# Performance work log

Measured on AMD Instinct MI355X. Metric: run time of the kernel, lower is better.

The kernel has to match this reference:

```python
import jax, jax.numpy as jnp
import numpy as np

B, S, D, H, L, V = 2, 2048, 1024, 16, 4, 2000
DK = D // H
DFF = 4 * D
EPS = 1e-5


def _pos_encoding(s, d):
    pos = np.arange(s, dtype=np.float64)[:, None]
    i = np.arange(d, dtype=np.float64)[None, :]
    angle = pos / np.power(10000.0, (i - (i % 2)) / d)
    pe = np.where(i % 2 == 0, np.sin(angle), np.cos(angle))
    return jnp.asarray(pe, jnp.float32)  # [S, D]


def setup_inputs() -> dict:
    key = jax.random.key(0)
    ks = jax.random.split(key, 12)
    sc = 0.02
    return {
        "indices": jax.random.randint(ks[0], (B, S), 0, V),
        "emb": jax.random.normal(ks[1], (V, D), jnp.float32) * sc,
        "Wq": jax.random.normal(ks[2], (L, H, DK, D), jnp.float32) * sc,
        "Wk": jax.random.normal(ks[3], (L, H, DK, D), jnp.float32) * sc,
        "Wv": jax.random.normal(ks[4], (L, H, DK, D), jnp.float32) * sc,
        "Wo": jax.random.normal(ks[5], (L, D, D), jnp.float32) * sc,
        "ln1_w": jnp.ones((L, D), jnp.float32),
        "ln1_b": jnp.zeros((L, D), jnp.float32),
        "W1": jax.random.normal(ks[6], (L, DFF, D), jnp.float32) * sc,
        "W2": jax.random.normal(ks[7], (L, D, DFF), jnp.float32) * sc,
        "ln2_w": jnp.ones((L, D), jnp.float32),
        "ln2_b": jnp.zeros((L, D), jnp.float32),
        "Wout": jax.random.normal(ks[8], (V, D), jnp.float32) * sc,
    }


def _layernorm(x, w, b):
    m = jnp.mean(x, axis=-1, keepdims=True)
    v = jnp.mean(jnp.square(x - m), axis=-1, keepdims=True)
    return (x - m) * jax.lax.rsqrt(v + EPS) * w + b


def reference(indices, emb, Wq, Wk, Wv, Wo, ln1_w, ln1_b, W1, W2, ln2_w, ln2_b, Wout):
    x = emb[indices] + _pos_encoding(S, D)  # [B, S, D]
    causal = jnp.tril(jnp.ones((S, S), bool))
    inv_sqrt_dk = 1.0 / np.sqrt(DK)
    for l in range(L):
        # per-head QKV projections, vectorized over heads
        q = jnp.einsum("bsd,hkd->bhsk", x, Wq[l])
        k = jnp.einsum("bsd,hkd->bhsk", x, Wk[l])
        v = jnp.einsum("bsd,hkd->bhsk", x, Wv[l])
        scores = jnp.einsum("bhqk,bhmk->bhqm", q, k) * inv_sqrt_dk
        scores = jnp.where(causal, scores, -jnp.inf)
        attn = jax.nn.softmax(scores, axis=-1)
        o = jnp.einsum("bhqm,bhmk->bhqk", attn, v)
        o = o.transpose(0, 2, 1, 3).reshape(B, S, D)  # concat heads
        o = o @ Wo[l].T
        x = _layernorm(x + o, ln1_w[l], ln1_b[l])
        h = jax.nn.relu(x @ W1[l].T) @ W2[l].T
        x = _layernorm(x + h, ln2_w[l], ln2_b[l])
    return x @ Wout.T  # [B, S, V]
```

## Files before the change

kernel.cpp:

```cpp
#include <hip/hip_runtime.h>
#include <hip/hip_bf16.h>

#define B_   2
#define S_   2048
#define D_   1024
#define H_   16
#define L_   4
#define DK_  64
#define DFF_ 4096
#define V_   2000

typedef __bf16 bf16x8 __attribute__((ext_vector_type(8)));
typedef float  f32x4  __attribute__((ext_vector_type(4)));
typedef __attribute__((address_space(1))) const void* as1cv;
typedef __attribute__((address_space(3))) void* as3v;

__device__ __forceinline__ void async_copy16(const void* g, void* l) {
    __builtin_amdgcn_global_load_lds((as1cv)g, (as3v)l, 16, 0, 0);
}

__global__ __launch_bounds__(256)
void canon_k(const void* __restrict__ src, __hip_bfloat16* __restrict__ dst,
             long n, const unsigned short* __restrict__ probe)
{
    const bool isbf = (probe[0] == 0x3F80u);
    long i0 = ((long)blockIdx.x * 256 + threadIdx.x) * 8;
    if (isbf) {
        const __hip_bfloat16* s = (const __hip_bfloat16*)src;
        #pragma unroll
        for (int j = 0; j < 8; ++j) {
            long i = i0 + j;
            if (i < n) dst[i] = s[i];
        }
    } else {
        const float* s = (const float*)src;
        #pragma unroll
        for (int j = 0; j < 8; ++j) {
            long i = i0 + j;
            if (i < n) dst[i] = __float2bfloat16(s[i]);
        }
    }
}

template<int MODE, int BN = 128>
__global__ __launch_bounds__(256, 2)
void gemm_bt(const __hip_bfloat16* __restrict__ A,
             const __hip_bfloat16* __restrict__ Wa,
             const __hip_bfloat16* __restrict__ Wb,
             const __hip_bfloat16* __restrict__ Wc,
             void* __restrict__ Oa, void* __restrict__ Obp, void* __restrict__ Ocp,
             const __hip_bfloat16* __restrict__ Res,
             const unsigned short* __restrict__ probe,
             int M, int N, int K)
{
    constexpr int NFR = BN / 32;

    const __hip_bfloat16* W = Wa;
    void* Out = Oa;
    if (blockIdx.z == 1) { W = Wb; Out = Obp; }
    else if (blockIdx.z == 2) { W = Wc; Out = Ocp; }

    __shared__ __bf16 As[2][128 * 32];
    __shared__ __bf16 Bs[2][BN * 32];

    const int tid  = threadIdx.x;
    const int wave = tid >> 6;
    const int lane = tid & 63;
    const int quad = lane >> 4;
    const int l16  = lane & 15;
    const int bm = blockIdx.x;
    const int bn = blockIdx.y;
    const int wm = (wave >> 1) * 64;
    const int wn = (wave & 1) * (BN / 2);

    const int sr = tid >> 2;
    const int sc = (tid & 3) * 8;
    const __hip_bfloat16* ap0 = A + (long)(bm * 128 + sr) * K + sc;
    const __hip_bfloat16* ap1 = ap0 + (long)64 * K;
    const __hip_bfloat16* bp0 = W + (long)(bn * BN + sr) * K + sc;
    const __hip_bfloat16* bp1 = bp0 + (long)64 * K;
    const bool bok0 = (bn * BN + sr) < N;
    const bool bok1 = (BN == 128) && (bn * BN + sr + 64) < N;

    if (N % BN) {
        #pragma unroll
        for (int bi = 0; bi < 2; ++bi)
            for (int c = tid; c < BN * 4; c += 256)
                ((bf16x8*)Bs[bi])[c] = (bf16x8)0;
        __syncthreads();
    }

    f32x4 acc[4][NFR] = {};
    const int nsteps = K >> 5;

    async_copy16(ap0, As[0] + wave * 512);
    async_copy16(ap1, As[0] + 2048 + wave * 512);
    if (bok0) async_copy16(bp0, Bs[0] + wave * 512);
    if constexpr (BN == 128) { if (bok1) async_copy16(bp1, Bs[0] + 2048 + wave * 512); }
    __syncthreads();

    int cur = 0;
    for (int t = 0; t < nsteps; ++t) {
        const int nxt = cur ^ 1;
        if (t + 1 < nsteps) {
            const int k0 = (t + 1) << 5;
            async_copy16(ap0 + k0, As[nxt] + wave * 512);
            async_copy16(ap1 + k0, As[nxt] + 2048 + wave * 512);
            if (bok0) async_copy16(bp0 + k0, Bs[nxt] + wave * 512);
            if constexpr (BN == 128) { if (bok1) async_copy16(bp1 + k0, Bs[nxt] + 2048 + wave * 512); }
        }

        bf16x8 af[4], bfr[NFR];
        #pragma unroll
        for (int i = 0; i < 4; ++i)
            af[i] = *(const bf16x8*)(As[cur] + (wm + i * 16 + l16) * 32 + quad * 8);
        #pragma unroll
        for (int i = 0; i < NFR; ++i)
            bfr[i] = *(const bf16x8*)(Bs[cur] + (wn + i * 16 + l16) * 32 + quad * 8);
        #pragma unroll
        for (int i = 0; i < 4; ++i)
            #pragma unroll
            for (int j = 0; j < NFR; ++j)
                acc[i][j] = __builtin_amdgcn_mfma_f32_16x16x32_bf16(af[i], bfr[j], acc[i][j], 0, 0, 0);

        __syncthreads();
        cur = nxt;
    }

    const bool out_bf = (MODE != 1) && (MODE != 3 || probe[0] == 0x3F80u);
    #pragma unroll
    for (int i = 0; i < 4; ++i) {
        #pragma unroll
        for (int r = 0; r < 4; ++r) {
            const long row = bm * 128 + wm + i * 16 + quad * 4 + r;
            #pragma unroll
            for (int j = 0; j < NFR; ++j) {
                const int col = bn * BN + wn + j * 16 + l16;
                if (col < N) {
                    const long idx = row * (long)N + col;
                    float v = acc[i][j][r];
                    if constexpr (MODE == 1) {
                        ((float*)Out)[idx] = v + __bfloat162float(Res[idx]);
                    } else if constexpr (MODE == 2) {
                        ((__hip_bfloat16*)Out)[idx] = __float2bfloat16(v > 0.f ? v : 0.f);
                    } else {
                        if (out_bf) ((__hip_bfloat16*)Out)[idx] = __float2bfloat16(v);
                        else        ((float*)Out)[idx] = v;
                    }
                }
            }
        }
    }
}

__global__ __launch_bounds__(256, 2)
void flash_attn(const __hip_bfloat16* __restrict__ Qg,
                const __hip_bfloat16* __restrict__ Kg,
                const __hip_bfloat16* __restrict__ Vg,
                __hip_bfloat16* __restrict__ Og)
{
    const int gid = blockIdx.x + 16 * (blockIdx.y + 16 * blockIdx.z);
    const int r8   = gid & 7;
    const int q9   = gid >> 3;
    const int bx   = q9 & 15;
    const int grp  = r8 + 8 * (q9 >> 4);
    const int h  = grp & 15;
    const int b  = grp >> 4;

    const int tid  = threadIdx.x;
    const int wave = tid >> 6;
    const int lane = tid & 63;
    const int quad = lane >> 4;
    const int l16  = lane & 15;

    __shared__ __bf16 Qs[64 * 64];
    __shared__ __bf16 Ks[2][64 * 64];
    __shared__ __bf16 Vs[64 * 64];
    __shared__ __bf16 Vt[64 * 72];
    __shared__ __bf16 Ps[4][16 * 72];

    const long base = ((long)b * S_) * D_ + (long)h * DK_;
    const int sr  = tid >> 3;
    const int scq = ((tid & 7) ^ (sr & 7)) * 8;
    const int scv = (tid & 7) * 8;

    for (int pr = 0; pr < 2; ++pr) {
        const int qt = pr ? (31 - bx) : bx;
        const int ntile = qt + 1;

        const __hip_bfloat16* qp = Qg + base + (long)(qt * 64 + sr) * D_ + scq;
        async_copy16(qp,           Qs + wave * 512);
        async_copy16(qp + 32 * D_, Qs + 2048 + wave * 512);
        {
            const __hip_bfloat16* kp = Kg + base + (long)sr * D_ + scq;
            const __hip_bfloat16* vp = Vg + base + (long)sr * D_ + scv;
            async_copy16(kp,           Ks[0] + wave * 512);
            async_copy16(kp + 32 * D_, Ks[0] + 2048 + wave * 512);
            async_copy16(vp,           Vs + wave * 512);
            async_copy16(vp + 32 * D_, Vs + 2048 + wave * 512);
        }
        __syncthreads();

        const int qr = wave * 16 + l16;
        const __bf16* qrow = Qs + qr * 64;
        bf16x8 qf0 = *(const bf16x8*)(qrow + (( quad      ^ (qr & 7)) * 8));
        bf16x8 qf1 = *(const bf16x8*)(qrow + (((quad + 4) ^ (qr & 7)) * 8));
        #pragma unroll
        for (int j = 0; j < 8; ++j) {
            qf0[j] = (__bf16)((float)qf0[j] * 0.125f);
            qf1[j] = (__bf16)((float)qf1[j] * 0.125f);
        }

        f32x4 o_acc[4] = {};
        float m_run[4], l_run[4];
        #pragma unroll
        for (int rr = 0; rr < 4; ++rr) { m_run[rr] = -1e30f; l_run[rr] = 0.f; }

        const int q_base = qt * 64 + wave * 16 + quad * 4;

        for (int it = 0; it < ntile; ++it) {
            const int cur = it & 1;
            const int kv0 = it * 64;
            const bool more = (it + 1 < ntile);

            if (more) {
                const __hip_bfloat16* kp = Kg + base + (long)(kv0 + 64 + sr) * D_ + scq;
                async_copy16(kp,           Ks[cur ^ 1] + wave * 512);
                async_copy16(kp + 32 * D_, Ks[cur ^ 1] + 2048 + wave * 512);
            }

            #pragma unroll
            for (int i = 0; i < 2; ++i) {
                const int seg = i * 256 + tid;
                const int dk  = seg & 63;
                const int kvc = (seg >> 6) * 8;
                bf16x8 t;
                #pragma unroll
                for (int j = 0; j < 8; ++j) t[j] = Vs[(kvc + j) * 64 + dk];
                *(bf16x8*)(Vt + dk * 72 + kvc) = t;
            }

            f32x4 sAcc[4] = {};
            #pragma unroll
            for (int nt = 0; nt < 4; ++nt) {
                const int kr = nt * 16 + l16;
                const __bf16* krow = Ks[cur] + kr * 64;
                const bf16x8 kf0 = *(const bf16x8*)(krow + (( quad      ^ (kr & 7)) * 8));
                const bf16x8 kf1 = *(const bf16x8*)(krow + (((quad + 4) ^ (kr & 7)) * 8));
                sAcc[nt] = __builtin_amdgcn_mfma_f32_16x16x32_bf16(qf0, kf0, sAcc[nt], 0, 0, 0);
                sAcc[nt] = __builtin_amdgcn_mfma_f32_16x16x32_bf16(qf1, kf1, sAcc[nt], 0, 0, 0);
            }

            float rmax[4];
            #pragma unroll
            for (int rr = 0; rr < 4; ++rr) rmax[rr] = -1e30f;
            if (kv0 == qt * 64) {
                #pragma unroll
                for (int nt = 0; nt < 4; ++nt)
                    #pragma unroll
                    for (int rr = 0; rr < 4; ++rr) {
                        float s = sAcc[nt][rr];
                        if ((kv0 + nt * 16 + l16) > (q_base + rr)) s = -1e30f;
                        sAcc[nt][rr] = s;
                        rmax[rr] = fmaxf(rmax[rr], s);
                    }
            } else {
                #pragma unroll
                for (int nt = 0; nt < 4; ++nt)
                    #pragma unroll
                    for (int rr = 0; rr < 4; ++rr)
                        rmax[rr] = fmaxf(rmax[rr], sAcc[nt][rr]);
            }
            #pragma unroll
            for (int off = 1; off < 16; off <<= 1)
                #pragma unroll
                for (int rr = 0; rr < 4; ++rr)
                    rmax[rr] = fmaxf(rmax[rr], __shfl_xor(rmax[rr], off, 64));

            float alpha[4], rsum[4];
            #pragma unroll
            for (int rr = 0; rr < 4; ++rr) {
                const float mn = fmaxf(m_run[rr], rmax[rr]);
                alpha[rr] = __expf(m_run[rr] - mn);
                m_run[rr] = mn;
                rsum[rr] = 0.f;
            }
            #pragma unroll
            for (int nt = 0; nt < 4; ++nt)
                #pragma unroll
                for (int rr = 0; rr < 4; ++rr) {
                    const float p = __expf(sAcc[nt][rr] - m_run[rr]);
                    sAcc[nt][rr] = p;
                    rsum[rr] += p;
                }
            #pragma unroll
            for (int off = 1; off < 16; off <<= 1)
                #pragma unroll
                for (int rr = 0; rr < 4; ++rr)
                    rsum[rr] += __shfl_xor(rsum[rr], off, 64);
            #pragma unroll
            for (int rr = 0; rr < 4; ++rr) l_run[rr] = l_run[rr] * alpha[rr] + rsum[rr];
            #pragma unroll
            for (int nt = 0; nt < 4; ++nt)
                #pragma unroll
                for (int rr = 0; rr < 4; ++rr) o_acc[nt][rr] *= alpha[rr];

            __bf16* pw = &Ps[wave][0];
            #pragma unroll
            for (int nt = 0; nt < 4; ++nt)
                #pragma unroll
                for (int rr = 0; rr < 4; ++rr)
                    pw[(quad * 4 + rr) * 72 + nt * 16 + l16] = (__bf16)sAcc[nt][rr];

            __syncthreads();

            if (more) {
                const __hip_bfloat16* vp = Vg + base + (long)(kv0 + 64 + sr) * D_ + scv;
                async_copy16(vp,           Vs + wave * 512);
                async_copy16(vp + 32 * D_, Vs + 2048 + wave * 512);
            }

            const __bf16* pb = pw + l16 * 72 + quad * 8;
            const bf16x8 pf0 = *(const bf16x8*)pb;
            const bf16x8 pf1 = *(const bf16x8*)(pb + 32);
            #pragma unroll
            for (int nt = 0; nt < 4; ++nt) {
                const __bf16* vb = Vt + (nt * 16 + l16) * 72 + quad * 8;
                o_acc[nt] = __builtin_amdgcn_mfma_f32_16x16x32_bf16(pf0, *(const bf16x8*)vb,        o_acc[nt], 0, 0, 0);
                o_acc[nt] = __builtin_amdgcn_mfma_f32_16x16x32_bf16(pf1, *(const bf16x8*)(vb + 32), o_acc[nt], 0, 0, 0);
            }

            __syncthreads();
        }

        #pragma unroll
        for (int nt = 0; nt < 4; ++nt)
            #pragma unroll
            for (int rr = 0; rr < 4; ++rr) {
                const long row = (long)b * S_ + qt * 64 + wave * 16 + quad * 4 + rr;
                const int col = h * DK_ + nt * 16 + l16;
                Og[row * D_ + col] = __float2bfloat16(o_acc[nt][rr] / l_run[rr]);
            }
    }
}

__global__ __launch_bounds__(256)
void layernorm_k(const float* __restrict__ in,
                 const __hip_bfloat16* __restrict__ w,
                 const __hip_bfloat16* __restrict__ bb,
                 __hip_bfloat16* __restrict__ out)
{
    const int row = blockIdx.x;
    const int tid = threadIdx.x;
    const float4 v = ((const float4*)(in + (long)row * D_))[tid];
    float s  = v.x + v.y + v.z + v.w;
    float ss = v.x * v.x + v.y * v.y + v.z * v.z + v.w * v.w;
    #pragma unroll
    for (int off = 1; off < 64; off <<= 1) {
        s  += __shfl_xor(s, off, 64);
        ss += __shfl_xor(ss, off, 64);
    }
    __shared__ float red[8];
    if ((tid & 63) == 0) { red[tid >> 6] = s; red[4 + (tid >> 6)] = ss; }
    __syncthreads();
    s  = red[0] + red[1] + red[2] + red[3];
    ss = red[4] + red[5] + red[6] + red[7];
    const float mean = s * (1.f / D_);
    const float var  = ss * (1.f / D_) - mean * mean;
    const float rs = rsqrtf(var + 1e-5f);
    const int d0 = tid * 4;
    const float xs[4] = { v.x, v.y, v.z, v.w };
    #pragma unroll
    for (int j = 0; j < 4; ++j) {
        const float wv = __bfloat162float(w[d0 + j]);
        const float bv = __bfloat162float(bb[d0 + j]);
        out[(long)row * D_ + d0 + j] = __float2bfloat16((xs[j] - mean) * rs * wv + bv);
    }
}

__global__ __launch_bounds__(256)
void embed_k(const int* __restrict__ idx,
             const __hip_bfloat16* __restrict__ emb,
             __hip_bfloat16* __restrict__ X)
{
    const int row = blockIdx.x;
    const int s = row & (S_ - 1);
    const int tid = threadIdx.x;
    const int token = idx[row];
    const __hip_bfloat16* e = emb + (long)token * D_;
    #pragma unroll
    for (int j = 0; j < 4; ++j) {
        const int d = tid + j * 256;
        const float di = (float)(d & ~1);
        const float freq = __expf(di * (-9.210340371976184f / (float)D_));
        const float angle = (float)s * freq;
        const float pe = (d & 1) ? cosf(angle) : sinf(angle);
        X[(long)row * D_ + d] = __float2bfloat16(__bfloat162float(e[d]) + pe);
    }
}

extern "C" void kernel_launch(void* const* d_in, const int* in_sizes, int n_in,
                              void* d_out, int out_size, void* d_ws, size_t ws_size,
                              hipStream_t stream)
{
    const int* indices = (const int*)d_in[0];
    const unsigned short* probe = (const unsigned short*)d_in[6];

    const long NTOK = (long)B_ * S_;
    char* ws = (char*)d_ws;
    __hip_bfloat16* X  = (__hip_bfloat16*)ws; ws += NTOK * D_ * 2;
    __hip_bfloat16* Qb = (__hip_bfloat16*)ws; ws += NTOK * D_ * 2;
    __hip_bfloat16* Kb = (__hip_bfloat16*)ws; ws += NTOK * D_ * 2;
    __hip_bfloat16* Vb = (__hip_bfloat16*)ws; ws += NTOK * D_ * 2;
    __hip_bfloat16* Ob = (__hip_bfloat16*)ws; ws += NTOK * D_ * 2;
    __hip_bfloat16* Hb = Qb;
    float* tmp = (float*)ws;                  ws += NTOK * D_ * 4;
    __hip_bfloat16* cEmb  = (__hip_bfloat16*)ws; ws += (long)V_ * D_ * 2;
    __hip_bfloat16* cWq   = (__hip_bfloat16*)ws; ws += (long)L_ * D_ * D_ * 2;
    __hip_bfloat16* cWk   = (__hip_bfloat16*)ws; ws += (long)L_ * D_ * D_ * 2;
    __hip_bfloat16* cWv   = (__hip_bfloat16*)ws; ws += (long)L_ * D_ * D_ * 2;
    __hip_bfloat16* cWo   = (__hip_bfloat16*)ws; ws += (long)L_ * D_ * D_ * 2;
    __hip_bfloat16* cW1   = (__hip_bfloat16*)ws; ws += (long)L_ * DFF_ * D_ * 2;
    __hip_bfloat16* cW2   = (__hip_bfloat16*)ws; ws += (long)L_ * D_ * DFF_ * 2;
    __hip_bfloat16* cWout = (__hip_bfloat16*)ws; ws += (long)V_ * D_ * 2;
    __hip_bfloat16* cLn1w = (__hip_bfloat16*)ws; ws += (long)L_ * D_ * 2;
    __hip_bfloat16* cLn1b = (__hip_bfloat16*)ws; ws += (long)L_ * D_ * 2;
    __hip_bfloat16* cLn2w = (__hip_bfloat16*)ws; ws += (long)L_ * D_ * 2;
    __hip_bfloat16* cLn2b = (__hip_bfloat16*)ws; ws += (long)L_ * D_ * 2;

    struct { const void* src; __hip_bfloat16* dst; long n; } cv[12] = {
        { d_in[1],  cEmb,  (long)V_ * D_ },
        { d_in[2],  cWq,   (long)L_ * D_ * D_ },
        { d_in[3],  cWk,   (long)L_ * D_ * D_ },
        { d_in[4],  cWv,   (long)L_ * D_ * D_ },
        { d_in[5],  cWo,   (long)L_ * D_ * D_ },
        { d_in[6],  cLn1w, (long)L_ * D_ },
        { d_in[7],  cLn1b, (long)L_ * D_ },
        { d_in[8],  cW1,   (long)L_ * DFF_ * D_ },
        { d_in[9],  cW2,   (long)L_ * D_ * DFF_ },
        { d_in[10], cLn2w, (long)L_ * D_ },
        { d_in[11], cLn2b, (long)L_ * D_ },
        { d_in[12], cWout, (long)V_ * D_ },
    };
    for (int i = 0; i < 12; ++i) {
        const long blocks = (cv[i].n + 2047) / 2048;
        canon_k<<<dim3((unsigned)blocks), 256, 0, stream>>>(cv[i].src, cv[i].dst, cv[i].n, probe);
    }

    embed_k<<<dim3(NTOK), 256, 0, stream>>>(indices, cEmb, X);

    for (int l = 0; l < L_; ++l) {
        const __hip_bfloat16* wq = cWq + (long)l * D_ * D_;
        const __hip_bfloat16* wk = cWk + (long)l * D_ * D_;
        const __hip_bfloat16* wv = cWv + (long)l * D_ * D_;
        const __hip_bfloat16* wo = cWo + (long)l * D_ * D_;
        const __hip_bfloat16* w1 = cW1 + (long)l * DFF_ * D_;
        const __hip_bfloat16* w2 = cW2 + (long)l * D_ * DFF_;

        gemm_bt<0><<<dim3(32, 8, 3), 256, 0, stream>>>(X, wq, wk, wv, Qb, Kb, Vb, nullptr, nullptr, 4096, 1024, 1024);
        flash_attn<<<dim3(16, 16, 2), 256, 0, stream>>>(Qb, Kb, Vb, Ob);
        gemm_bt<1, 64><<<dim3(32, 16, 1), 256, 0, stream>>>(Ob, wo, wo, wo, tmp, tmp, tmp, X, nullptr, 4096, 1024, 1024);
        layernorm_k<<<dim3(4096), 256, 0, stream>>>(tmp, cLn1w + l * D_, cLn1b + l * D_, X);
        gemm_bt<2><<<dim3(32, 32, 1), 256, 0, stream>>>(X, w1, w1, w1, Hb, Hb, Hb, nullptr, nullptr, 4096, 4096, 1024);
        gemm_bt<1, 64><<<dim3(32, 16, 1), 256, 0, stream>>>(Hb, w2, w2, w2, tmp, tmp, tmp, X, nullptr, 4096, 1024, 4096);
        layernorm_k<<<dim3(4096), 256, 0, stream>>>(tmp, cLn2w + l * D_, cLn2b + l * D_, X);
    }

    gemm_bt<3><<<dim3(32, 16, 1), 256, 0, stream>>>(X, cWout, cWout, cWout, d_out, d_out, d_out, nullptr, probe, 4096, V_, 1024);
}
```

Measured before the change: 1.475 ms.

## Split flash attention into one block per query tile with smaller LDS

```diff
diff --git a/kernel.cpp b/kernel.cpp
--- a/kernel.cpp
+++ b/kernel.cpp
@@ -159,13 +159,16 @@
                 const __hip_bfloat16* __restrict__ Vg,
                 __hip_bfloat16* __restrict__ Og)
 {
-    const int gid = blockIdx.x + 16 * (blockIdx.y + 16 * blockIdx.z);
-    const int r8   = gid & 7;
-    const int q9   = gid >> 3;
-    const int bx   = q9 & 15;
-    const int grp  = r8 + 8 * (q9 >> 4);
-    const int h  = grp & 15;
-    const int b  = grp >> 4;
+    const int gid = blockIdx.x;
+    const int xcd = gid & 7;
+    const int s9  = gid >> 3;
+    const int q5  = s9 & 31;
+    const int w2  = s9 >> 5;
+    const int a   = q5 >> 1;
+    const int qt  = (w2 & 1) ? (31 - a) : a;
+    const int grp = xcd + 8 * ((q5 & 1) | ((w2 >> 1) << 1));
+    const int h = grp & 15;
+    const int b = grp >> 4;
 
     const int tid  = threadIdx.x;
     const int wave = tid >> 6;
@@ -173,10 +176,9 @@
     const int quad = lane >> 4;
     const int l16  = lane & 15;
 
-    __shared__ __bf16 Qs[64 * 64];
-    __shared__ __bf16 Ks[2][64 * 64];
+    __shared__ __bf16 QVt[64 * 72];
+    __shared__ __bf16 Ks[64 * 64];
     __shared__ __bf16 Vs[64 * 64];
-    __shared__ __bf16 Vt[64 * 72];
     __shared__ __bf16 Ps[4][16 * 72];
 
     const long base = ((long)b * S_) * D_ + (long)h * DK_;
@@ -184,164 +186,159 @@
     const int scq = ((tid & 7) ^ (sr & 7)) * 8;
     const int scv = (tid & 7) * 8;
 
-    for (int pr = 0; pr < 2; ++pr) {
-        const int qt = pr ? (31 - bx) : bx;
-        const int ntile = qt + 1;
-
-        const __hip_bfloat16* qp = Qg + base + (long)(qt * 64 + sr) * D_ + scq;
-        async_copy16(qp,           Qs + wave * 512);
-        async_copy16(qp + 32 * D_, Qs + 2048 + wave * 512);
-        {
-            const __hip_bfloat16* kp = Kg + base + (long)sr * D_ + scq;
-            const __hip_bfloat16* vp = Vg + base + (long)sr * D_ + scv;
-            async_copy16(kp,           Ks[0] + wave * 512);
-            async_copy16(kp + 32 * D_, Ks[0] + 2048 + wave * 512);
-            async_copy16(vp,           Vs + wave * 512);
-            async_copy16(vp + 32 * D_, Vs + 2048 + wave * 512);
-        }
-        __syncthreads();
-
-        const int qr = wave * 16 + l16;
-        const __bf16* qrow = Qs + qr * 64;
-        bf16x8 qf0 = *(const bf16x8*)(qrow + (( quad      ^ (qr & 7)) * 8));
-        bf16x8 qf1 = *(const bf16x8*)(qrow + (((quad + 4) ^ (qr & 7)) * 8));
-        #pragma unroll
-        for (int j = 0; j < 8; ++j) {
-            qf0[j] = (__bf16)((float)qf0[j] * 0.125f);
-            qf1[j] = (__bf16)((float)qf1[j] * 0.125f);
-        }
-
-        f32x4 o_acc[4] = {};
-        float m_run[4], l_run[4];
-        #pragma unroll
-        for (int rr = 0; rr < 4; ++rr) { m_run[rr] = -1e30f; l_run[rr] = 0.f; }
-
-        const int q_base = qt * 64 + wave * 16 + quad * 4;
-
-        for (int it = 0; it < ntile; ++it) {
-            const int cur = it & 1;
-            const int kv0 = it * 64;
-            const bool more = (it + 1 < ntile);
-
-            if (more) {
-                const __hip_bfloat16* kp = Kg + base + (long)(kv0 + 64 + sr) * D_ + scq;
-                async_copy16(kp,           Ks[cur ^ 1] + wave * 512);
-                async_copy16(kp + 32 * D_, Ks[cur ^ 1] + 2048 + wave * 512);
-            }
-
-            #pragma unroll
-            for (int i = 0; i < 2; ++i) {
-                const int seg = i * 256 + tid;
-                const int dk  = seg & 63;
-                const int kvc = (seg >> 6) * 8;
-                bf16x8 t;
-                #pragma unroll
-                for (int j = 0; j < 8; ++j) t[j] = Vs[(kvc + j) * 64 + dk];
-                *(bf16x8*)(Vt + dk * 72 + kvc) = t;
-            }
-
-            f32x4 sAcc[4] = {};
-            #pragma unroll
-            for (int nt = 0; nt < 4; ++nt) {
-                const int kr = nt * 16 + l16;
-                const __bf16* krow = Ks[cur] + kr * 64;
-                const bf16x8 kf0 = *(const bf16x8*)(krow + (( quad      ^ (kr & 7)) * 8));
-                const bf16x8 kf1 = *(const bf16x8*)(krow + (((quad + 4) ^ (kr & 7)) * 8));
-                sAcc[nt] = __builtin_amdgcn_mfma_f32_16x16x32_bf16(qf0, kf0, sAcc[nt], 0, 0, 0);
-                sAcc[nt] = __builtin_amdgcn_mfma_f32_16x16x32_bf16(qf1, kf1, sAcc[nt], 0, 0, 0);
-            }
-
-            float rmax[4];
-            #pragma unroll
-            for (int rr = 0; rr < 4; ++rr) rmax[rr] = -1e30f;
-            if (kv0 == qt * 64) {
-                #pragma unroll
-                for (int nt = 0; nt < 4; ++nt)
-                    #pragma unroll
-                    for (int rr = 0; rr < 4; ++rr) {
-                        float s = sAcc[nt][rr];
-                        if ((kv0 + nt * 16 + l16) > (q_base + rr)) s = -1e30f;
-                        sAcc[nt][rr] = s;
-                        rmax[rr] = fmaxf(rmax[rr], s);
-                    }
-            } else {
-                #pragma unroll
-                for (int nt = 0; nt < 4; ++nt)
-                    #pragma unroll
-                    for (int rr = 0; rr < 4; ++rr)
-                        rmax[rr] = fmaxf(rmax[rr], sAcc[nt][rr]);
-            }
-            #pragma unroll
-            for (int off = 1; off < 16; off <<= 1)
-                #pragma unroll
-                for (int rr = 0; rr < 4; ++rr)
-                    rmax[rr] = fmaxf(rmax[rr], __shfl_xor(rmax[rr], off, 64));
-
-            float alpha[4], rsum[4];
-            #pragma unroll
-            for (int rr = 0; rr < 4; ++rr) {
-                const float mn = fmaxf(m_run[rr], rmax[rr]);
-                alpha[rr] = __expf(m_run[rr] - mn);
-                m_run[rr] = mn;
-                rsum[rr] = 0.f;
-            }
+    const int ntile = qt + 1;
+
+    const __hip_bfloat16* qp = Qg + base + (long)(qt * 64 + sr) * D_ + scq;
+    async_copy16(qp,           QVt + wave * 512);
+    async_copy16(qp + 32 * D_, QVt + 2048 + wave * 512);
+    {
+        const __hip_bfloat16* kp = Kg + base + (long)sr * D_ + scq;
+        const __hip_bfloat16* vp = Vg + base + (long)sr * D_ + scv;
+        async_copy16(kp,           Ks + wave * 512);
+        async_copy16(kp + 32 * D_, Ks + 2048 + wave * 512);
+        async_copy16(vp,           Vs + wave * 512);
+        async_copy16(vp + 32 * D_, Vs + 2048 + wave * 512);
+    }
+    __syncthreads();
+
+    const int qr = wave * 16 + l16;
+    const __bf16* qrow = QVt + qr * 64;
+    bf16x8 qf0 = *(const bf16x8*)(qrow + (( quad      ^ (qr & 7)) * 8));
+    bf16x8 qf1 = *(const bf16x8*)(qrow + (((quad + 4) ^ (qr & 7)) * 8));
+    #pragma unroll
+    for (int j = 0; j < 8; ++j) {
+        qf0[j] = (__bf16)((float)qf0[j] * 0.125f);
+        qf1[j] = (__bf16)((float)qf1[j] * 0.125f);
+    }
+    __syncthreads();
+
+    f32x4 o_acc[4] = {};
+    float m_run[4], l_run[4];
+    #pragma unroll
+    for (int rr = 0; rr < 4; ++rr) { m_run[rr] = -1e30f; l_run[rr] = 0.f; }
+
+    const int q_base = qt * 64 + wave * 16 + quad * 4;
+
+    for (int it = 0; it < ntile; ++it) {
+        const int kv0 = it * 64;
+        const bool more = (it + 1 < ntile);
+
+        __bf16* Vt = QVt;
+        #pragma unroll
+        for (int i = 0; i < 2; ++i) {
+            const int seg = i * 256 + tid;
+            const int dk  = seg & 63;
+            const int kvc = (seg >> 6) * 8;
+            bf16x8 t;
+            #pragma unroll
+            for (int j = 0; j < 8; ++j) t[j] = Vs[(kvc + j) * 64 + dk];
+            *(bf16x8*)(Vt + dk * 72 + kvc) = t;
+        }
+
+        f32x4 sAcc[4] = {};
+        #pragma unroll
+        for (int nt = 0; nt < 4; ++nt) {
+            const int kr = nt * 16 + l16;
+            const __bf16* krow = Ks + kr * 64;
+            const bf16x8 kf0 = *(const bf16x8*)(krow + (( quad      ^ (kr & 7)) * 8));
+            const bf16x8 kf1 = *(const bf16x8*)(krow + (((quad + 4) ^ (kr & 7)) * 8));
+            sAcc[nt] = __builtin_amdgcn_mfma_f32_16x16x32_bf16(qf0, kf0, sAcc[nt], 0, 0, 0);
+            sAcc[nt] = __builtin_amdgcn_mfma_f32_16x16x32_bf16(qf1, kf1, sAcc[nt], 0, 0, 0);
+        }
+
+        float rmax[4];
+        #pragma unroll
+        for (int rr = 0; rr < 4; ++rr) rmax[rr] = -1e30f;
+        if (kv0 == qt * 64) {
             #pragma unroll
             for (int nt = 0; nt < 4; ++nt)
                 #pragma unroll
                 for (int rr = 0; rr < 4; ++rr) {
-                    const float p = __expf(sAcc[nt][rr] - m_run[rr]);
-                    sAcc[nt][rr] = p;
-                    rsum[rr] += p;
+                    float s = sAcc[nt][rr];
+                    if ((kv0 + nt * 16 + l16) > (q_base + rr)) s = -1e30f;
+                    sAcc[nt][rr] = s;
+                    rmax[rr] = fmaxf(rmax[rr], s);
                 }
-            #pragma unroll
-            for (int off = 1; off < 16; off <<= 1)
-                #pragma unroll
-                for (int rr = 0; rr < 4; ++rr)
-                    rsum[rr] += __shfl_xor(rsum[rr], off, 64);
-            #pragma unroll
-            for (int rr = 0; rr < 4; ++rr) l_run[rr] = l_run[rr] * alpha[rr] + rsum[rr];
-            #pragma unroll
-            for (int nt = 0; nt < 4; ++nt)
-                #pragma unroll
-                for (int rr = 0; rr < 4; ++rr) o_acc[nt][rr] *= alpha[rr];
-
-            __bf16* pw = &Ps[wave][0];
+        } else {
             #pragma unroll
             for (int nt = 0; nt < 4; ++nt)
                 #pragma unroll
                 for (int rr = 0; rr < 4; ++rr)
-                    pw[(quad * 4 + rr) * 72 + nt * 16 + l16] = (__bf16)sAcc[nt][rr];
-
-            __syncthreads();
-
-            if (more) {
-                const __hip_bfloat16* vp = Vg + base + (long)(kv0 + 64 + sr) * D_ + scv;
-                async_copy16(vp,           Vs + wave * 512);
-                async_copy16(vp + 32 * D_, Vs + 2048 + wave * 512);
+                    rmax[rr] = fmaxf(rmax[rr], sAcc[nt][rr]);
+        }
+        #pragma unroll
+        for (int off = 1; off < 16; off <<= 1)
+            #pragma unroll
+            for (int rr = 0; rr < 4; ++rr)
+                rmax[rr] = fmaxf(rmax[rr], __shfl_xor(rmax[rr], off, 64));
+
+        float alpha[4], rsum[4];
+        #pragma unroll
+        for (int rr = 0; rr < 4; ++rr) {
+            const float mn = fmaxf(m_run[rr], rmax[rr]);
+            alpha[rr] = __expf(m_run[rr] - mn);
+            m_run[rr] = mn;
+            rsum[rr] = 0.f;
+        }
+        #pragma unroll
+        for (int nt = 0; nt < 4; ++nt)
+            #pragma unroll
+            for (int rr = 0; rr < 4; ++rr) {
+                const float p = __expf(sAcc[nt][rr] - m_run[rr]);
+                sAcc[nt][rr] = p;
+                rsum[rr] += p;
             }
-
-            const __bf16* pb = pw + l16 * 72 + quad * 8;
-            const bf16x8 pf0 = *(const bf16x8*)pb;
-            const bf16x8 pf1 = *(const bf16x8*)(pb + 32);
-            #pragma unroll
-            for (int nt = 0; nt < 4; ++nt) {
-                const __bf16* vb = Vt + (nt * 16 + l16) * 72 + quad * 8;
-                o_acc[nt] = __builtin_amdgcn_mfma_f32_16x16x32_bf16(pf0, *(const bf16x8*)vb,        o_acc[nt], 0, 0, 0);
-                o_acc[nt] = __builtin_amdgcn_mfma_f32_16x16x32_bf16(pf1, *(const bf16x8*)(vb + 32), o_acc[nt], 0, 0, 0);
-            }
-
-            __syncthreads();
-        }
-
+        #pragma unroll
+        for (int off = 1; off < 16; off <<= 1)
+            #pragma unroll
+            for (int rr = 0; rr < 4; ++rr)
+                rsum[rr] += __shfl_xor(rsum[rr], off, 64);
+        #pragma unroll
+        for (int rr = 0; rr < 4; ++rr) l_run[rr] = l_run[rr] * alpha[rr] + rsum[rr];
         #pragma unroll
         for (int nt = 0; nt < 4; ++nt)
             #pragma unroll
-            for (int rr = 0; rr < 4; ++rr) {
-                const long row = (long)b * S_ + qt * 64 + wave * 16 + quad * 4 + rr;
-                const int col = h * DK_ + nt * 16 + l16;
-                Og[row * D_ + col] = __float2bfloat16(o_acc[nt][rr] / l_run[rr]);
-            }
-    }
+            for (int rr = 0; rr < 4; ++rr) o_acc[nt][rr] *= alpha[rr];
+
+        __bf16* pw = &Ps[wave][0];
+        #pragma unroll
+        for (int nt = 0; nt < 4; ++nt)
+            #pragma unroll
+            for (int rr = 0; rr < 4; ++rr)
+                pw[(quad * 4 + rr) * 72 + nt * 16 + l16] = (__bf16)sAcc[nt][rr];
+
+        __syncthreads();
+
+        if (more) {
+            const __hip_bfloat16* kp = Kg + base + (long)(kv0 + 64 + sr) * D_ + scq;
+            const __hip_bfloat16* vp = Vg + base + (long)(kv0 + 64 + sr) * D_ + scv;
+            async_copy16(kp,           Ks + wave * 512);
+            async_copy16(kp + 32 * D_, Ks + 2048 + wave * 512);
+            async_copy16(vp,           Vs + wave * 512);
+            async_copy16(vp + 32 * D_, Vs + 2048 + wave * 512);
+        }
+
+        const __bf16* pb = pw + l16 * 72 + quad * 8;
+        const bf16x8 pf0 = *(const bf16x8*)pb;
+        const bf16x8 pf1 = *(const bf16x8*)(pb + 32);
+        #pragma unroll
+        for (int nt = 0; nt < 4; ++nt) {
+            const __bf16* vb = QVt + (nt * 16 + l16) * 72 + quad * 8;
+            o_acc[nt] = __builtin_amdgcn_mfma_f32_16x16x32_bf16(pf0, *(const bf16x8*)vb,        o_acc[nt], 0, 0, 0);
+            o_acc[nt] = __builtin_amdgcn_mfma_f32_16x16x32_bf16(pf1, *(const bf16x8*)(vb + 32), o_acc[nt], 0, 0, 0);
+        }
+
+        __syncthreads();
+    }
+
+    #pragma unroll
+    for (int nt = 0; nt < 4; ++nt)
+        #pragma unroll
+        for (int rr = 0; rr < 4; ++rr) {
+            const long row = (long)b * S_ + qt * 64 + wave * 16 + quad * 4 + rr;
+            const int col = h * DK_ + nt * 16 + l16;
+            Og[row * D_ + col] = __float2bfloat16(o_acc[nt][rr] / l_run[rr]);
+        }
 }
 
 __global__ __launch_bounds__(256)
@@ -458,7 +455,7 @@
         const __hip_bfloat16* w2 = cW2 + (long)l * D_ * DFF_;
 
         gemm_bt<0><<<dim3(32, 8, 3), 256, 0, stream>>>(X, wq, wk, wv, Qb, Kb, Vb, nullptr, nullptr, 4096, 1024, 1024);
-        flash_attn<<<dim3(16, 16, 2), 256, 0, stream>>>(Qb, Kb, Vb, Ob);
+        flash_attn<<<dim3(1024), 256, 0, stream>>>(Qb, Kb, Vb, Ob);
         gemm_bt<1, 64><<<dim3(32, 16, 1), 256, 0, stream>>>(Ob, wo, wo, wo, tmp, tmp, tmp, X, nullptr, 4096, 1024, 1024);
         layernorm_k<<<dim3(4096), 256, 0, stream>>>(tmp, cLn1w + l * D_, cLn1b + l * D_, X);
         gemm_bt<2><<<dim3(32, 32, 1), 256, 0, stream>>>(X, w1, w1, w1, Hb, Hb, Hb, nullptr, nullptr, 4096, 4096, 1024);
```

Measured after the change: 1.544 ms. +4.7%, slower.
